# Performance work log

Measured on AMD Instinct MI355X. Metric: run time of the kernel, lower is better.

## Reference

```python
import jax, jax.numpy as jnp
import numpy as np

B, HH, WW, C = 8, 128, 128, 128
NH = 4          # total heads; each branch uses NH//2
SS = 2          # split_size
EPS = 1e-5


def setup_inputs() -> dict:
    key = jax.random.key(0)
    ks = jax.random.split(key, 10)
    Ch = C // 2
    Dff = 4 * C
    return {
        "x": jax.random.normal(ks[0], (B, HH * WW, C), jnp.float32),
        "ln1_g": jnp.ones((C,), jnp.float32),
        "ln1_b": jnp.zeros((C,), jnp.float32),
        "w_qkv": jax.random.normal(ks[1], (3 * C, C), jnp.float32) * 0.02,
        "w_proj": jax.random.normal(ks[2], (C, C), jnp.float32) * 0.02,
        "b_proj": jnp.zeros((C,), jnp.float32),
        "conv_w0": jax.random.normal(ks[3], (Ch, 1, 3, 3), jnp.float32) * 0.02,
        "conv_b0": jnp.zeros((Ch,), jnp.float32),
        "conv_w1": jax.random.normal(ks[4], (Ch, 1, 3, 3), jnp.float32) * 0.02,
        "conv_b1": jnp.zeros((Ch,), jnp.float32),
        "ln2_g": jnp.ones((C,), jnp.float32),
        "ln2_b": jnp.zeros((C,), jnp.float32),
        "w1": jax.random.normal(ks[5], (Dff, C), jnp.float32) * 0.02,
        "b1": jnp.zeros((Dff,), jnp.float32),
        "w2": jax.random.normal(ks[6], (C, Dff), jnp.float32) * 0.02,
        "b2": jnp.zeros((C,), jnp.float32),
        "H": HH,
        "W": WW,
    }


def _layernorm(x, g, b):
    m = jnp.mean(x, axis=-1, keepdims=True)
    v = jnp.mean(jnp.square(x - m), axis=-1, keepdims=True)
    return (x - m) * jax.lax.rsqrt(v + EPS) * g + b


def _cswin_branch(q, k, v, conv_w, conv_b, H, W, H_sp, W_sp, heads):
    """q,k,v: [B, H*W, Ch] -> [B, H*W, Ch] cross-shaped-window LePE attention."""
    Bq, L, Ch = q.shape
    hd = Ch // heads
    T = H_sp * W_sp
    nh, nw = H // H_sp, W // W_sp

    def to_win(t):  # [B,L,Ch] -> [nW*B, heads, T, hd]
        t = t.reshape(Bq, nh, H_sp, nw, W_sp, Ch).transpose(0, 1, 3, 2, 4, 5)
        return t.reshape(-1, T, heads, hd).transpose(0, 2, 1, 3)

    qw, kw = to_win(q), to_win(k)

    # v as window images [nW*B, Ch, H_sp, W_sp] for depthwise LePE conv
    vimg = v.reshape(Bq, nh, H_sp, nw, W_sp, Ch).transpose(0, 1, 3, 5, 2, 4)
    vimg = vimg.reshape(-1, Ch, H_sp, W_sp)
    lepe = jax.lax.conv_general_dilated(
        vimg, conv_w, window_strides=(1, 1), padding="SAME",
        feature_group_count=Ch,
        dimension_numbers=("NCHW", "OIHW", "NCHW"),
    ) + conv_b[None, :, None, None]
    lepe = lepe.reshape(-1, heads, hd, T).transpose(0, 1, 3, 2)  # [nW*B,h,T,hd]
    vw = vimg.reshape(-1, heads, hd, T).transpose(0, 1, 3, 2)

    scale = hd ** -0.5
    attn = jnp.einsum("whtd,whsd->whts", qw * scale, kw)
    attn = jax.nn.softmax(attn, axis=-1)
    out = jnp.einsum("whts,whsd->whtd", attn, vw) + lepe  # [nW*B,h,T,hd]

    out = out.transpose(0, 2, 1, 3).reshape(-1, T, Ch)
    out = out.reshape(Bq, nh, nw, H_sp, W_sp, Ch).transpose(0, 1, 3, 2, 4, 5)
    return out.reshape(Bq, H * W, Ch)


def reference(x, ln1_g, ln1_b, w_qkv, w_proj, b_proj, conv_w0, conv_b0,
              conv_w1, conv_b1, ln2_g, ln2_b, w1, b1, w2, b2, H, W):
    Bx, L, Cx = x.shape
    Ch = Cx // 2
    heads = NH // 2

    img = _layernorm(x, ln1_g, ln1_b)
    qkv = (img @ w_qkv.T).reshape(Bx, L, 3, Cx)
    q, k, v = qkv[:, :, 0, :], qkv[:, :, 1, :], qkv[:, :, 2, :]

    # idx=0: horizontal stripes (H_sp=H, W_sp=SS); idx=1: vertical (H_sp=SS, W_sp=W)
    x1 = _cswin_branch(q[..., :Ch], k[..., :Ch], v[..., :Ch],
                       conv_w0, conv_b0, H, W, H, SS, heads)
    x2 = _cswin_branch(q[..., Ch:], k[..., Ch:], v[..., Ch:],
                       conv_w1, conv_b1, H, W, SS, W, heads)
    att = jnp.concatenate([x1, x2], axis=2)
    att = att @ w_proj.T + b_proj

    x = x + att
    h = _layernorm(x, ln2_g, ln2_b)
    h = jax.nn.gelu(h @ w1.T + b1, approximate=False) @ w2.T + b2
    return x + h
```

## Files before the change

### kernel.cpp

```cpp
#include <hip/hip_runtime.h>
#include <cstddef>


#define LDIM 16384
#define NTOK 131072
#define PLANE ((size_t)NTOK * 128)

typedef __attribute__((ext_vector_type(8))) short bf16x8;
typedef __attribute__((ext_vector_type(4))) float f32x4;

__device__ __forceinline__ unsigned short f2bf(float f) {
  union { float f; unsigned int i; } u; u.f = f;
  unsigned int r = u.i + 0x7fffu + ((u.i >> 16) & 1u);
  return (unsigned short)(r >> 16);
}
__device__ __forceinline__ float bflo(unsigned int u) {
  union { unsigned int i; float f; } x; x.i = u << 16; return x.f;
}
__device__ __forceinline__ float bfhi(unsigned int u) {
  union { unsigned int i; float f; } x; x.i = u & 0xffff0000u; return x.f;
}
__device__ __forceinline__ unsigned int pk(float a, float b) {
  return (unsigned)f2bf(a) | ((unsigned)f2bf(b) << 16);
}

__device__ __forceinline__ void async16(const unsigned short* g, unsigned short* l) {
  __builtin_amdgcn_global_load_lds(
      (const __attribute__((address_space(1))) unsigned int*)g,
      (__attribute__((address_space(3))) unsigned int*)l, 16, 0, 0);
}

__device__ __forceinline__ void wait_lgkm0() {
  asm volatile("s_waitcnt lgkmcnt(0)" ::: "memory");
  __builtin_amdgcn_sched_barrier(0);
}
__device__ __forceinline__ void wait_vm0() {
  asm volatile("s_waitcnt vmcnt(0)" ::: "memory");
  __builtin_amdgcn_sched_barrier(0);
}
__device__ __forceinline__ void barrier_lgkm() {
  asm volatile("s_waitcnt lgkmcnt(0)" ::: "memory");
  __builtin_amdgcn_s_barrier();
  __builtin_amdgcn_sched_barrier(0);
}

__device__ __forceinline__ bf16x8 fragS(const unsigned short* base, int row, int c) {
  return *(const bf16x8*)(base + row * 128 + ((c ^ (row & 7)) << 3));
}

__device__ __forceinline__ void stageS128(const unsigned short* __restrict__ src, int rowStride,
                                          unsigned short* dst, int tid) {
  const int lane = tid & 63, wv = tid >> 6;
  #pragma unroll
  for (int i = 0; i < 8; i++) {
    const int base = i * 256 + wv * 64;
    const int f = base + lane;
    const int row = f >> 4, cs = f & 15, cg = cs ^ (row & 7);
    async16(src + (size_t)row * rowStride + (cg << 3), dst + (size_t)base * 8);
  }
}

__device__ __forceinline__ void stageS64(const unsigned short* __restrict__ src,
                                         unsigned short* dst, int tid) {
  const int lane = tid & 63, wv = tid >> 6;
  #pragma unroll
  for (int i = 0; i < 4; i++) {
    const int base = i * 256 + wv * 64;
    const int f = base + lane;
    const int row = f >> 4, cs = f & 15, cg = cs ^ (row & 7);
    async16(src + (size_t)row * 128 + (cg << 3), dst + (size_t)base * 8);
  }
}

__device__ __forceinline__ void stageW32(const unsigned short* __restrict__ src, int rowStride,
                                         unsigned short* dstRegion, int lane) {
  #pragma unroll
  for (int i = 0; i < 8; i++) {
    const int rowLocal = i * 4 + (lane >> 4);
    const int cs = lane & 15, cg = cs ^ (rowLocal & 7);
    async16(src + (size_t)rowLocal * rowStride + (cg << 3), dstRegion + i * 512);
  }
}

__device__ __forceinline__ void gemmS(const unsigned short* As, const unsigned short* Bs,
                                      f32x4 acc[4][4], int wm, int wn, int q, int r) {
  #pragma unroll
  for (int kc = 0; kc < 4; kc++) {
    bf16x8 a[4], b[4];
    #pragma unroll
    for (int mt = 0; mt < 4; mt++) a[mt] = fragS(As, wm * 64 + mt * 16 + r, kc * 4 + q);
    #pragma unroll
    for (int nt = 0; nt < 4; nt++) b[nt] = fragS(Bs, wn * 64 + nt * 16 + r, kc * 4 + q);
    #pragma unroll
    for (int mt = 0; mt < 4; mt++)
      #pragma unroll
      for (int nt = 0; nt < 4; nt++)
        acc[mt][nt] = __builtin_amdgcn_mfma_f32_16x16x32_bf16(a[mt], b[nt], acc[mt][nt], 0, 0, 0);
  }
}

__device__ __forceinline__ void storeC(f32x4 acc[4][4], unsigned short* Cs,
                                       unsigned short* __restrict__ dst, int dstStride, int tid) {
  const int wv = tid >> 6, lane = tid & 63, q = lane >> 4, r = lane & 15;
  const int wm = wv & 1, wn = wv >> 1;
  #pragma unroll
  for (int mt = 0; mt < 4; mt++)
    #pragma unroll
    for (int nt = 0; nt < 4; nt++) {
      const int col = wn * 64 + nt * 16 + r;
      #pragma unroll
      for (int rg = 0; rg < 4; rg++) {
        const int row = wm * 64 + mt * 16 + q * 4 + rg;
        Cs[row * 128 + ((((col >> 3) ^ (row & 7)) << 3) | (col & 7))] = f2bf(acc[mt][nt][rg]);
      }
    }
  __syncthreads();
  #pragma unroll
  for (int i = 0; i < 8; i++) {
    const int f = tid + i * 256;
    const int row = f >> 4, cs = f & 15, cg = cs ^ (row & 7);
    *(uint4*)(dst + (size_t)row * dstStride + (cg << 3)) = *(const uint4*)(Cs + row * 128 + cs * 8);
  }
}

__device__ __forceinline__ float gelu_t(float x) {
  const float y = -2.3022083f * (x + 0.044715f * x * x * x);
  const float p = __builtin_amdgcn_exp2f(y);
  return x * __builtin_amdgcn_rcpf(1.f + p);
}

__global__ void k_prep(const float* __restrict__ wq, const float* __restrict__ wp,
                       const float* __restrict__ w1, const float* __restrict__ w2,
                       unsigned short* __restrict__ wb)
{
  const int id = blockIdx.x * 256 + threadIdx.x;
  const float* src; int off;
  if (id < 12288)      { src = wq; off = id; }
  else if (id < 16384) { src = wp; off = id - 12288; }
  else if (id < 32768) { src = w1; off = id - 16384; }
  else                 { src = w2; off = id - 32768; }
  const float4 v = *(const float4*)(src + (size_t)off * 4);
  uint2 u; u.x = pk(v.x, v.y); u.y = pk(v.z, v.w);
  *(uint2*)(wb + (size_t)id * 4) = u;
}

__global__ __launch_bounds__(256, 2) void k_ln_qkv(
    const float* __restrict__ x, const float* __restrict__ g, const float* __restrict__ bb,
    const unsigned short* __restrict__ wqkvb, unsigned short* __restrict__ qkv)
{
  __shared__ unsigned short xs[128 * 128];
  __shared__ unsigned short ws[128 * 128];
  __shared__ float redS[128][2], redQ[128][2];
  const int tid = threadIdx.x;
  const long m0 = (long)blockIdx.x * 128;
  {
    const int m = tid >> 1, hf = tid & 1;
    const float4* xg = (const float4*)(x + (size_t)(m0 + m) * 128 + hf * 64);
    float4 xv[16];
    #pragma unroll
    for (int i = 0; i < 16; i++) xv[i] = xg[i];
    float s1 = 0.f, s2 = 0.f;
    #pragma unroll
    for (int i = 0; i < 16; i++) {
      s1 += xv[i].x + xv[i].y + xv[i].z + xv[i].w;
      s2 += xv[i].x * xv[i].x + xv[i].y * xv[i].y + xv[i].z * xv[i].z + xv[i].w * xv[i].w;
    }
    redS[m][hf] = s1; redQ[m][hf] = s2;
    __syncthreads();
    const float mean = (redS[m][0] + redS[m][1]) * (1.f / 128.f);
    const float var  = (redQ[m][0] + redQ[m][1]) * (1.f / 128.f) - mean * mean;
    const float rs = rsqrtf(var + 1e-5f);
    const float4* g4 = (const float4*)(g + hf * 64);
    const float4* b4 = (const float4*)(bb + hf * 64);
    #pragma unroll
    for (int i = 0; i < 8; i++) {
      float4 v0 = xv[2 * i], v1 = xv[2 * i + 1];
      float4 g0 = g4[2 * i], g1 = g4[2 * i + 1], p0 = b4[2 * i], p1 = b4[2 * i + 1];
      uint4 u;
      u.x = pk((v0.x - mean) * rs * g0.x + p0.x, (v0.y - mean) * rs * g0.y + p0.y);
      u.y = pk((v0.z - mean) * rs * g0.z + p0.z, (v0.w - mean) * rs * g0.w + p0.w);
      u.z = pk((v1.x - mean) * rs * g1.x + p1.x, (v1.y - mean) * rs * g1.y + p1.y);
      u.w = pk((v1.z - mean) * rs * g1.z + p1.z, (v1.w - mean) * rs * g1.w + p1.w);
      const int c = hf * 8 + i;
      *(uint4*)&xs[m * 128 + ((c ^ (m & 7)) << 3)] = u;
    }
  }
  const int lane = tid & 63, q = lane >> 4, r = lane & 15;
  const int wv = tid >> 6, wm = wv & 1, wn = wv >> 1;
  for (int nc = 0; nc < 3; nc++) {
    __syncthreads();
    stageS128(wqkvb + (size_t)nc * 16384, 128, ws, tid);
    __syncthreads();
    f32x4 acc[4][4];
    #pragma unroll
    for (int a = 0; a < 4; a++)
      #pragma unroll
      for (int b = 0; b < 4; b++) acc[a][b] = f32x4{0.f, 0.f, 0.f, 0.f};
    gemmS(xs, ws, acc, wm, wn, q, r);
    __syncthreads();
    storeC(acc, ws, qkv + (size_t)nc * PLANE + (size_t)m0 * 128, 128, tid);
  }
}

__global__ __launch_bounds__(256, 2) void k_attn(
    const unsigned short* __restrict__ qkv,
    const float* __restrict__ conv_w0, const float* __restrict__ conv_b0,
    const float* __restrict__ conv_w1, const float* __restrict__ conv_b1,
    unsigned short* __restrict__ att)
{
  __shared__ unsigned short Kt[256][40];
  __shared__ unsigned short Vt[32][264];
  __shared__ unsigned short Ps[4][64][72];
  const unsigned short* kpl = qkv + PLANE;
  const unsigned short* vpl = qkv + 2 * PLANE;
  const int t = threadIdx.x;
  const int win = blockIdx.x, head = blockIdx.y, br = blockIdx.z;
  const int bimg = win >> 6, widx = win & 63;
  const int c0 = br * 64 + head * 32;
  const int lgWs = (br == 0) ? 1 : 7;
  const int Wsm1 = (1 << lgWs) - 1;
  const long base = (long)bimg * LDIM + ((br == 0) ? widx * 2 : widx * 256);

  {
    const long tj = base + (long)(t >> lgWs) * 128 + (t & Wsm1);
    const uint4* kp = (const uint4*)(kpl + (size_t)tj * 128 + c0);
    uint4 k0v = kp[0], k1v = kp[1], k2v = kp[2], k3v = kp[3];
    *(uint4*)&Kt[t][0]  = k0v;  *(uint4*)&Kt[t][8]  = k1v;
    *(uint4*)&Kt[t][16] = k2v;  *(uint4*)&Kt[t][24] = k3v;
    const uint4* vp = (const uint4*)(vpl + (size_t)tj * 128 + c0);
    uint4 vv[4] = {vp[0], vp[1], vp[2], vp[3]};
    const unsigned short* vs = (const unsigned short*)vv;
    #pragma unroll
    for (int d = 0; d < 32; d++) Vt[d][t] = vs[d];
  }
  const int wave = t >> 6, lane = t & 63, q = lane >> 4, r = lane & 15;
  const int qbase = wave * 64;
  bf16x8 qf[4];
  #pragma unroll
  for (int mt = 0; mt < 4; mt++) {
    const int row = qbase + mt * 16 + r;
    const long tok = base + (long)(row >> lgWs) * 128 + (row & Wsm1);
    qf[mt] = *(const bf16x8*)(qkv + (size_t)tok * 128 + c0 + q * 8);
  }
  __syncthreads();

  const float factor = 0.17677669529663687f * 1.44269504088896341f;
  f32x4 Oacc[4][2];
  float psum[4][4];
  #pragma unroll
  for (int mt = 0; mt < 4; mt++) {
    Oacc[mt][0] = f32x4{0.f, 0.f, 0.f, 0.f};
    Oacc[mt][1] = f32x4{0.f, 0.f, 0.f, 0.f};
    #pragma unroll
    for (int rg = 0; rg < 4; rg++) psum[mt][rg] = 0.f;
  }

  for (int kc = 0; kc < 4; kc++) {
    bf16x8 kb[4];
    #pragma unroll
    for (int nt = 0; nt < 4; nt++) kb[nt] = *(const bf16x8*)&Kt[kc * 64 + nt * 16 + r][q * 8];
    f32x4 s[4][4];
    #pragma unroll
    for (int mt = 0; mt < 4; mt++)
      #pragma unroll
      for (int nt = 0; nt < 4; nt++) {
        f32x4 z = f32x4{0.f, 0.f, 0.f, 0.f};
        s[mt][nt] = __builtin_amdgcn_mfma_f32_16x16x32_bf16(qf[mt], kb[nt], z, 0, 0, 0);
      }
    #pragma unroll
    for (int mt = 0; mt < 4; mt++)
      #pragma unroll
      for (int nt = 0; nt < 4; nt++)
        #pragma unroll
        for (int rg = 0; rg < 4; rg++) {
          const float p = __builtin_amdgcn_exp2f(s[mt][nt][rg] * factor);
          psum[mt][rg] += p;
          Ps[wave][mt * 16 + q * 4 + rg][nt * 16 + r] = f2bf(p);
        }
    #pragma unroll
    for (int kst = 0; kst < 2; kst++) {
      bf16x8 pa[4], vb[2];
      #pragma unroll
      for (int mt = 0; mt < 4; mt++) pa[mt] = *(const bf16x8*)&Ps[wave][mt * 16 + r][kst * 32 + q * 8];
      #pragma unroll
      for (int nto = 0; nto < 2; nto++) vb[nto] = *(const bf16x8*)&Vt[nto * 16 + r][kc * 64 + kst * 32 + q * 8];
      #pragma unroll
      for (int mt = 0; mt < 4; mt++)
        #pragma unroll
        for (int nto = 0; nto < 2; nto++)
          Oacc[mt][nto] = __builtin_amdgcn_mfma_f32_16x16x32_bf16(pa[mt], vb[nto], Oacc[mt][nto], 0, 0, 0);
    }
  }

  #pragma unroll
  for (int mt = 0; mt < 4; mt++)
    #pragma unroll
    for (int rg = 0; rg < 4; rg++) {
      float v = psum[mt][rg];
      v += __shfl_xor(v, 1); v += __shfl_xor(v, 2);
      v += __shfl_xor(v, 4); v += __shfl_xor(v, 8);
      psum[mt][rg] = __builtin_amdgcn_rcpf(v);
    }

  const float* cw = br ? conv_w1 : conv_w0;
  const float* cb = br ? conv_b1 : conv_b0;
  float wle[2][9], ble[2];
  #pragma unroll
  for (int nto = 0; nto < 2; nto++) {
    const int ch = head * 32 + nto * 16 + r;
    ble[nto] = cb[ch];
    #pragma unroll
    for (int tp = 0; tp < 9; tp++) wle[nto][tp] = cw[ch * 9 + tp];
  }
  const int WsW = 1 << lgWs;
  const int HsW = 256 >> lgWs;

  #pragma unroll
  for (int mt = 0; mt < 4; mt++)
    #pragma unroll
    for (int rg = 0; rg < 4; rg++) {
      const int row = qbase + mt * 16 + q * 4 + rg;
      const int ii = row >> lgWs, jj = row & Wsm1;
      const long tok = base + (long)ii * 128 + jj;
      float lep0 = ble[0], lep1 = ble[1];
      #pragma unroll
      for (int di = -1; di <= 1; di++) {
        if ((unsigned)(ii + di) >= (unsigned)HsW) continue;
        #pragma unroll
        for (int dj = -1; dj <= 1; dj++) {
          if ((unsigned)(jj + dj) >= (unsigned)WsW) continue;
          const int nb = row + di * WsW + dj;
          const int tap = (di + 1) * 3 + (dj + 1);
          lep0 = fmaf(bflo(Vt[r][nb]),      wle[0][tap], lep0);
          lep1 = fmaf(bflo(Vt[16 + r][nb]), wle[1][tap], lep1);
        }
      }
      const float pr = psum[mt][rg];
      att[(size_t)tok * 128 + c0 + r]      = f2bf(Oacc[mt][0][rg] * pr + lep0);
      att[(size_t)tok * 128 + c0 + 16 + r] = f2bf(Oacc[mt][1][rg] * pr + lep1);
    }
}

__global__ __launch_bounds__(256, 2) void k_projmlp(
    const unsigned short* __restrict__ att, const unsigned short* __restrict__ wprojb,
    const float* __restrict__ b_proj, const float* __restrict__ x,
    const float* __restrict__ g, const float* __restrict__ bb,
    const unsigned short* __restrict__ w1b, const unsigned short* __restrict__ w2b,
    const float* __restrict__ b1, const float* __restrict__ b2,
    float* __restrict__ out)
{
  __shared__ unsigned short hs[64 * 128];
  __shared__ unsigned short xs[64 * 128];
  __shared__ unsigned short ws[128 * 128];
  __shared__ float redS[64][4], redQ[64][4];
  const int tid = threadIdx.x;
  const long m0 = (long)blockIdx.x * 64;
  const int lane = tid & 63, q = lane >> 4, r = lane & 15, wv = tid >> 6;
  unsigned short* wsW = ws + (size_t)wv * 32 * 128;

  stageS64(att + (size_t)m0 * 128, hs, tid);
  stageW32(wprojb + (size_t)(wv * 32) * 128, 128, wsW, lane);

  float xv[4][2][4];
  #pragma unroll
  for (int mt = 0; mt < 4; mt++)
    #pragma unroll
    for (int nt = 0; nt < 2; nt++) {
      const int col = wv * 32 + nt * 16 + r;
      #pragma unroll
      for (int rg = 0; rg < 4; rg++)
        xv[mt][nt][rg] = x[(size_t)(m0 + mt * 16 + q * 4 + rg) * 128 + col];
    }
  float bpv[2], gv[2], bv2[2], b1v[4][2], b2v[2];
  #pragma unroll
  for (int nt = 0; nt < 2; nt++) {
    const int col = wv * 32 + nt * 16 + r;
    bpv[nt] = b_proj[col]; gv[nt] = g[col]; bv2[nt] = bb[col]; b2v[nt] = b2[col];
    #pragma unroll
    for (int nc = 0; nc < 4; nc++) b1v[nc][nt] = b1[nc * 128 + col];
  }
  __syncthreads();

  f32x4 xres[4][2];
  #pragma unroll
  for (int mt = 0; mt < 4; mt++) { xres[mt][0] = f32x4{0.f,0.f,0.f,0.f}; xres[mt][1] = f32x4{0.f,0.f,0.f,0.f}; }
  #pragma unroll
  for (int kc = 0; kc < 4; kc++) {
    bf16x8 a[4], b[2];
    #pragma unroll
    for (int mt = 0; mt < 4; mt++) a[mt] = fragS(hs, mt * 16 + r, kc * 4 + q);
    #pragma unroll
    for (int nt = 0; nt < 2; nt++) b[nt] = fragS(ws, wv * 32 + nt * 16 + r, kc * 4 + q);
    #pragma unroll
    for (int mt = 0; mt < 4; mt++)
      #pragma unroll
      for (int nt = 0; nt < 2; nt++)
        xres[mt][nt] = __builtin_amdgcn_mfma_f32_16x16x32_bf16(a[mt], b[nt], xres[mt][nt], 0, 0, 0);
  }
  wait_lgkm0();
  stageW32(w1b + (size_t)(wv * 32) * 128, 128, wsW, lane);

  #pragma unroll
  for (int mt = 0; mt < 4; mt++)
    #pragma unroll
    for (int nt = 0; nt < 2; nt++)
      #pragma unroll
      for (int rg = 0; rg < 4; rg++)
        xres[mt][nt][rg] += xv[mt][nt][rg] + bpv[nt];

  #pragma unroll
  for (int mt = 0; mt < 4; mt++)
    #pragma unroll
    for (int rg = 0; rg < 4; rg++) {
      float s1 = xres[mt][0][rg] + xres[mt][1][rg];
      float s2 = xres[mt][0][rg] * xres[mt][0][rg] + xres[mt][1][rg] * xres[mt][1][rg];
      s1 += __shfl_xor(s1, 1); s1 += __shfl_xor(s1, 2); s1 += __shfl_xor(s1, 4); s1 += __shfl_xor(s1, 8);
      s2 += __shfl_xor(s2, 1); s2 += __shfl_xor(s2, 2); s2 += __shfl_xor(s2, 4); s2 += __shfl_xor(s2, 8);
      if (r == 0) { const int row = mt * 16 + q * 4 + rg; redS[row][wv] = s1; redQ[row][wv] = s2; }
    }
  barrier_lgkm();
  #pragma unroll
  for (int mt = 0; mt < 4; mt++)
    #pragma unroll
    for (int rg = 0; rg < 4; rg++) {
      const int row = mt * 16 + q * 4 + rg;
      const float s1 = redS[row][0] + redS[row][1] + redS[row][2] + redS[row][3];
      const float s2 = redQ[row][0] + redQ[row][1] + redQ[row][2] + redQ[row][3];
      const float mean = s1 * (1.f / 128.f);
      const float var  = s2 * (1.f / 128.f) - mean * mean;
      const float rs = rsqrtf(var + 1e-5f);
      #pragma unroll
      for (int nt = 0; nt < 2; nt++) {
        const int col = wv * 32 + nt * 16 + r;
        const float v = (xres[mt][nt][rg] - mean) * rs * gv[nt] + bv2[nt];
        xs[row * 128 + ((((col >> 3) ^ (row & 7)) << 3) | (col & 7))] = f2bf(v);
      }
    }
  barrier_lgkm();

  f32x4 oacc[4][2];
  #pragma unroll
  for (int mt = 0; mt < 4; mt++) { oacc[mt][0] = f32x4{0.f,0.f,0.f,0.f}; oacc[mt][1] = f32x4{0.f,0.f,0.f,0.f}; }

  for (int nc = 0; nc < 4; nc++) {
    wait_vm0();
    bf16x8 b1f[4][2];
    #pragma unroll
    for (int kc = 0; kc < 4; kc++)
      #pragma unroll
      for (int nt = 0; nt < 2; nt++)
        b1f[kc][nt] = fragS(ws, wv * 32 + nt * 16 + r, kc * 4 + q);
    wait_lgkm0();
    stageW32(w2b + (size_t)(wv * 32) * 512 + nc * 128, 512, wsW, lane);
    f32x4 h[4][2];
    #pragma unroll
    for (int mt = 0; mt < 4; mt++) { h[mt][0] = f32x4{0.f,0.f,0.f,0.f}; h[mt][1] = f32x4{0.f,0.f,0.f,0.f}; }
    #pragma unroll
    for (int kc = 0; kc < 4; kc++) {
      bf16x8 a[4];
      #pragma unroll
      for (int mt = 0; mt < 4; mt++) a[mt] = fragS(xs, mt * 16 + r, kc * 4 + q);
      #pragma unroll
      for (int mt = 0; mt < 4; mt++)
        #pragma unroll
        for (int nt = 0; nt < 2; nt++)
          h[mt][nt] = __builtin_amdgcn_mfma_f32_16x16x32_bf16(a[mt], b1f[kc][nt], h[mt][nt], 0, 0, 0);
    }
    barrier_lgkm();
    #pragma unroll
    for (int mt = 0; mt < 4; mt++)
      #pragma unroll
      for (int nt = 0; nt < 2; nt++) {
        const int col = wv * 32 + nt * 16 + r;
        const float bv = b1v[nc][nt];
        #pragma unroll
        for (int rg = 0; rg < 4; rg++) {
          const int rw = mt * 16 + q * 4 + rg;
          hs[rw * 128 + ((((col >> 3) ^ (rw & 7)) << 3) | (col & 7))] = f2bf(gelu_t(h[mt][nt][rg] + bv));
        }
      }
    barrier_lgkm();
    wait_vm0();
    bf16x8 b2f[4][2];
    #pragma unroll
    for (int kc = 0; kc < 4; kc++)
      #pragma unroll
      for (int nt = 0; nt < 2; nt++)
        b2f[kc][nt] = fragS(ws, wv * 32 + nt * 16 + r, kc * 4 + q);
    wait_lgkm0();
    if (nc < 3)
      stageW32(w1b + (size_t)((nc + 1) * 128 + wv * 32) * 128, 128, wsW, lane);
    #pragma unroll
    for (int kc = 0; kc < 4; kc++) {
      bf16x8 a[4];
      #pragma unroll
      for (int mt = 0; mt < 4; mt++) a[mt] = fragS(hs, mt * 16 + r, kc * 4 + q);
      #pragma unroll
      for (int mt = 0; mt < 4; mt++)
        #pragma unroll
        for (int nt = 0; nt < 2; nt++)
          oacc[mt][nt] = __builtin_amdgcn_mfma_f32_16x16x32_bf16(a[mt], b2f[kc][nt], oacc[mt][nt], 0, 0, 0);
    }
  }
  #pragma unroll
  for (int mt = 0; mt < 4; mt++)
    #pragma unroll
    for (int nt = 0; nt < 2; nt++) {
      const float bv = b2v[nt];
      const int col = wv * 32 + nt * 16 + r;
      #pragma unroll
      for (int rg = 0; rg < 4; rg++) {
        const size_t idx = (size_t)(m0 + mt * 16 + q * 4 + rg) * 128 + col;
        out[idx] = xres[mt][nt][rg] + bv + oacc[mt][nt][rg];
      }
    }
}

extern "C" void kernel_launch(void* const* d_in, const int* in_sizes, int n_in,
                              void* d_out, int out_size, void* d_ws, size_t ws_size,
                              hipStream_t stream) {
  const float* x       = (const float*)d_in[0];
  const float* ln1_g   = (const float*)d_in[1];
  const float* ln1_b   = (const float*)d_in[2];
  const float* w_qkv   = (const float*)d_in[3];
  const float* w_proj  = (const float*)d_in[4];
  const float* b_proj  = (const float*)d_in[5];
  const float* conv_w0 = (const float*)d_in[6];
  const float* conv_b0 = (const float*)d_in[7];
  const float* conv_w1 = (const float*)d_in[8];
  const float* conv_b1 = (const float*)d_in[9];
  const float* ln2_g   = (const float*)d_in[10];
  const float* ln2_b   = (const float*)d_in[11];
  const float* w1      = (const float*)d_in[12];
  const float* b1      = (const float*)d_in[13];
  const float* w2      = (const float*)d_in[14];
  const float* b2      = (const float*)d_in[15];
  float* out = (float*)d_out;

  unsigned short* qkv = (unsigned short*)d_ws;
  unsigned short* att = qkv;
  unsigned short* wb  = qkv + 3 * PLANE;
  unsigned short* wqkvb  = wb;
  unsigned short* wprojb = wb + 49152;
  unsigned short* w1b    = wb + 65536;
  unsigned short* w2b    = wb + 131072;

  k_prep<<<dim3(192), 256, 0, stream>>>(w_qkv, w_proj, w1, w2, wb);
  k_ln_qkv<<<dim3(NTOK / 128), 256, 0, stream>>>(x, ln1_g, ln1_b, wqkvb, qkv);
  k_attn<<<dim3(512, 2, 2), 256, 0, stream>>>(qkv, conv_w0, conv_b0, conv_w1, conv_b1, att);
  k_projmlp<<<dim3(NTOK / 64), 256, 0, stream>>>(att, wprojb, b_proj, x, ln2_g, ln2_b,
                                                 w1b, w2b, b1, b2, out);
}
```

Measured before the change: 345.2 us.

## Pipeline per-wave QKV weight staging and add MFMA priority hints

Restructures the LN+QKV kernel so each wave stages only its own 32-row weight slice asynchronously. The first slice is prefetched before the layernorm, and the next slice loads while the current GEMM runs, replacing the block-wide stage/sync/gemm/storeC sequence. Outputs are written straight from registers as packed bf16 pairs, with no shared-memory epilogue. It also wraps MFMA loops in several kernels with s_setprio so matrix work gets issue priority. The cost is more accumulator registers (8x2 tiles per wave) and narrower, less coalesced global stores.

After: 358.2 us. 3.8% more time.

```diff
diff --git a/kernel.cpp b/kernel.cpp
--- a/kernel.cpp
+++ b/kernel.cpp
@@ -38,6 +38,10 @@
   asm volatile("s_waitcnt vmcnt(0)" ::: "memory");
   __builtin_amdgcn_sched_barrier(0);
 }
+__device__ __forceinline__ void wait_vm16() {
+  asm volatile("s_waitcnt vmcnt(16)" ::: "memory");
+  __builtin_amdgcn_sched_barrier(0);
+}
 __device__ __forceinline__ void barrier_lgkm() {
   asm volatile("s_waitcnt lgkmcnt(0)" ::: "memory");
   __builtin_amdgcn_s_barrier();
@@ -46,18 +50,6 @@
 
 __device__ __forceinline__ bf16x8 fragS(const unsigned short* base, int row, int c) {
   return *(const bf16x8*)(base + row * 128 + ((c ^ (row & 7)) << 3));
-}
-
-__device__ __forceinline__ void stageS128(const unsigned short* __restrict__ src, int rowStride,
-                                          unsigned short* dst, int tid) {
-  const int lane = tid & 63, wv = tid >> 6;
-  #pragma unroll
-  for (int i = 0; i < 8; i++) {
-    const int base = i * 256 + wv * 64;
-    const int f = base + lane;
-    const int row = f >> 4, cs = f & 15, cg = cs ^ (row & 7);
-    async16(src + (size_t)row * rowStride + (cg << 3), dst + (size_t)base * 8);
-  }
 }
 
 __device__ __forceinline__ void stageS64(const unsigned short* __restrict__ src,
@@ -79,47 +71,6 @@
     const int rowLocal = i * 4 + (lane >> 4);
     const int cs = lane & 15, cg = cs ^ (rowLocal & 7);
     async16(src + (size_t)rowLocal * rowStride + (cg << 3), dstRegion + i * 512);
-  }
-}
-
-__device__ __forceinline__ void gemmS(const unsigned short* As, const unsigned short* Bs,
-                                      f32x4 acc[4][4], int wm, int wn, int q, int r) {
-  #pragma unroll
-  for (int kc = 0; kc < 4; kc++) {
-    bf16x8 a[4], b[4];
-    #pragma unroll
-    for (int mt = 0; mt < 4; mt++) a[mt] = fragS(As, wm * 64 + mt * 16 + r, kc * 4 + q);
-    #pragma unroll
-    for (int nt = 0; nt < 4; nt++) b[nt] = fragS(Bs, wn * 64 + nt * 16 + r, kc * 4 + q);
-    #pragma unroll
-    for (int mt = 0; mt < 4; mt++)
-      #pragma unroll
-      for (int nt = 0; nt < 4; nt++)
-        acc[mt][nt] = __builtin_amdgcn_mfma_f32_16x16x32_bf16(a[mt], b[nt], acc[mt][nt], 0, 0, 0);
-  }
-}
-
-__device__ __forceinline__ void storeC(f32x4 acc[4][4], unsigned short* Cs,
-                                       unsigned short* __restrict__ dst, int dstStride, int tid) {
-  const int wv = tid >> 6, lane = tid & 63, q = lane >> 4, r = lane & 15;
-  const int wm = wv & 1, wn = wv >> 1;
-  #pragma unroll
-  for (int mt = 0; mt < 4; mt++)
-    #pragma unroll
-    for (int nt = 0; nt < 4; nt++) {
-      const int col = wn * 64 + nt * 16 + r;
-      #pragma unroll
-      for (int rg = 0; rg < 4; rg++) {
-        const int row = wm * 64 + mt * 16 + q * 4 + rg;
-        Cs[row * 128 + ((((col >> 3) ^ (row & 7)) << 3) | (col & 7))] = f2bf(acc[mt][nt][rg]);
-      }
-    }
-  __syncthreads();
-  #pragma unroll
-  for (int i = 0; i < 8; i++) {
-    const int f = tid + i * 256;
-    const int row = f >> 4, cs = f & 15, cg = cs ^ (row & 7);
-    *(uint4*)(dst + (size_t)row * dstStride + (cg << 3)) = *(const uint4*)(Cs + row * 128 + cs * 8);
   }
 }
 
@@ -153,6 +104,11 @@
   __shared__ float redS[128][2], redQ[128][2];
   const int tid = threadIdx.x;
   const long m0 = (long)blockIdx.x * 128;
+  const int lane = tid & 63, q = lane >> 4, r = lane & 15, wv = tid >> 6;
+  unsigned short* wsW = ws + (size_t)wv * 32 * 128;
+
+  stageW32(wqkvb + (size_t)(wv * 32) * 128, 128, wsW, lane);
+
   {
     const int m = tid >> 1, hf = tid & 1;
     const float4* xg = (const float4*)(x + (size_t)(m0 + m) * 128 + hf * 64);
@@ -166,7 +122,7 @@
       s2 += xv[i].x * xv[i].x + xv[i].y * xv[i].y + xv[i].z * xv[i].z + xv[i].w * xv[i].w;
     }
     redS[m][hf] = s1; redQ[m][hf] = s2;
-    __syncthreads();
+    barrier_lgkm();
     const float mean = (redS[m][0] + redS[m][1]) * (1.f / 128.f);
     const float var  = (redQ[m][0] + redQ[m][1]) * (1.f / 128.f) - mean * mean;
     const float rs = rsqrtf(var + 1e-5f);
@@ -185,20 +141,45 @@
       *(uint4*)&xs[m * 128 + ((c ^ (m & 7)) << 3)] = u;
     }
   }
-  const int lane = tid & 63, q = lane >> 4, r = lane & 15;
-  const int wv = tid >> 6, wm = wv & 1, wn = wv >> 1;
+  barrier_lgkm();
+
   for (int nc = 0; nc < 3; nc++) {
-    __syncthreads();
-    stageS128(wqkvb + (size_t)nc * 16384, 128, ws, tid);
-    __syncthreads();
-    f32x4 acc[4][4];
-    #pragma unroll
-    for (int a = 0; a < 4; a++)
-      #pragma unroll
-      for (int b = 0; b < 4; b++) acc[a][b] = f32x4{0.f, 0.f, 0.f, 0.f};
-    gemmS(xs, ws, acc, wm, wn, q, r);
-    __syncthreads();
-    storeC(acc, ws, qkv + (size_t)nc * PLANE + (size_t)m0 * 128, 128, tid);
+    if (nc == 0) wait_vm0(); else wait_vm16();
+    bf16x8 wf[4][2];
+    #pragma unroll
+    for (int kc = 0; kc < 4; kc++)
+      #pragma unroll
+      for (int nt = 0; nt < 2; nt++)
+        wf[kc][nt] = fragS(ws, wv * 32 + nt * 16 + r, kc * 4 + q);
+    wait_lgkm0();
+    if (nc < 2)
+      stageW32(wqkvb + (size_t)((nc + 1) * 128 + wv * 32) * 128, 128, wsW, lane);
+    f32x4 acc[8][2];
+    #pragma unroll
+    for (int mt = 0; mt < 8; mt++) { acc[mt][0] = f32x4{0.f,0.f,0.f,0.f}; acc[mt][1] = f32x4{0.f,0.f,0.f,0.f}; }
+    __builtin_amdgcn_s_setprio(1);
+    #pragma unroll
+    for (int kc = 0; kc < 4; kc++) {
+      bf16x8 xf[8];
+      #pragma unroll
+      for (int mt = 0; mt < 8; mt++) xf[mt] = fragS(xs, mt * 16 + r, kc * 4 + q);
+      #pragma unroll
+      for (int mt = 0; mt < 8; mt++)
+        #pragma unroll
+        for (int nt = 0; nt < 2; nt++)
+          acc[mt][nt] = __builtin_amdgcn_mfma_f32_16x16x32_bf16(wf[kc][nt], xf[mt], acc[mt][nt], 0, 0, 0);
+    }
+    __builtin_amdgcn_s_setprio(0);
+    unsigned short* dst = qkv + (size_t)nc * PLANE + (size_t)m0 * 128;
+    #pragma unroll
+    for (int mt = 0; mt < 8; mt++)
+      #pragma unroll
+      for (int nt = 0; nt < 2; nt++) {
+        uint2 u;
+        u.x = pk(acc[mt][nt][0], acc[mt][nt][1]);
+        u.y = pk(acc[mt][nt][2], acc[mt][nt][3]);
+        *(uint2*)(dst + (size_t)(mt * 16 + r) * 128 + wv * 32 + nt * 16 + q * 4) = u;
+      }
   }
 }
 
@@ -260,6 +241,7 @@
     #pragma unroll
     for (int nt = 0; nt < 4; nt++) kb[nt] = *(const bf16x8*)&Kt[kc * 64 + nt * 16 + r][q * 8];
     f32x4 s[4][4];
+    __builtin_amdgcn_s_setprio(1);
     #pragma unroll
     for (int mt = 0; mt < 4; mt++)
       #pragma unroll
@@ -267,6 +249,7 @@
         f32x4 z = f32x4{0.f, 0.f, 0.f, 0.f};
         s[mt][nt] = __builtin_amdgcn_mfma_f32_16x16x32_bf16(qf[mt], kb[nt], z, 0, 0, 0);
       }
+    __builtin_amdgcn_s_setprio(0);
     #pragma unroll
     for (int mt = 0; mt < 4; mt++)
       #pragma unroll
@@ -284,11 +267,13 @@
       for (int mt = 0; mt < 4; mt++) pa[mt] = *(const bf16x8*)&Ps[wave][mt * 16 + r][kst * 32 + q * 8];
       #pragma unroll
       for (int nto = 0; nto < 2; nto++) vb[nto] = *(const bf16x8*)&Vt[nto * 16 + r][kc * 64 + kst * 32 + q * 8];
+      __builtin_amdgcn_s_setprio(1);
       #pragma unroll
       for (int mt = 0; mt < 4; mt++)
         #pragma unroll
         for (int nto = 0; nto < 2; nto++)
           Oacc[mt][nto] = __builtin_amdgcn_mfma_f32_16x16x32_bf16(pa[mt], vb[nto], Oacc[mt][nto], 0, 0, 0);
+      __builtin_amdgcn_s_setprio(0);
     }
   }
 
@@ -384,6 +369,7 @@
   f32x4 xres[4][2];
   #pragma unroll
   for (int mt = 0; mt < 4; mt++) { xres[mt][0] = f32x4{0.f,0.f,0.f,0.f}; xres[mt][1] = f32x4{0.f,0.f,0.f,0.f}; }
+  __builtin_amdgcn_s_setprio(1);
   #pragma unroll
   for (int kc = 0; kc < 4; kc++) {
     bf16x8 a[4], b[2];
@@ -397,6 +383,7 @@
       for (int nt = 0; nt < 2; nt++)
         xres[mt][nt] = __builtin_amdgcn_mfma_f32_16x16x32_bf16(a[mt], b[nt], xres[mt][nt], 0, 0, 0);
   }
+  __builtin_amdgcn_s_setprio(0);
   wait_lgkm0();
   stageW32(w1b + (size_t)(wv * 32) * 128, 128, wsW, lane);
 
@@ -455,6 +442,7 @@
     f32x4 h[4][2];
     #pragma unroll
     for (int mt = 0; mt < 4; mt++) { h[mt][0] = f32x4{0.f,0.f,0.f,0.f}; h[mt][1] = f32x4{0.f,0.f,0.f,0.f}; }
+    __builtin_amdgcn_s_setprio(1);
     #pragma unroll
     for (int kc = 0; kc < 4; kc++) {
       bf16x8 a[4];
@@ -466,6 +454,7 @@
         for (int nt = 0; nt < 2; nt++)
           h[mt][nt] = __builtin_amdgcn_mfma_f32_16x16x32_bf16(a[mt], b1f[kc][nt], h[mt][nt], 0, 0, 0);
     }
+    __builtin_amdgcn_s_setprio(0);
     barrier_lgkm();
     #pragma unroll
     for (int mt = 0; mt < 4; mt++)
@@ -490,6 +479,7 @@
     wait_lgkm0();
     if (nc < 3)
       stageW32(w1b + (size_t)((nc + 1) * 128 + wv * 32) * 128, 128, wsW, lane);
+    __builtin_amdgcn_s_setprio(1);
     #pragma unroll
     for (int kc = 0; kc < 4; kc++) {
       bf16x8 a[4];
@@ -501,6 +491,7 @@
         for (int nt = 0; nt < 2; nt++)
           oacc[mt][nt] = __builtin_amdgcn_mfma_f32_16x16x32_bf16(a[mt], b2f[kc][nt], oacc[mt][nt], 0, 0, 0);
     }
+    __builtin_amdgcn_s_setprio(0);
   }
   #pragma unroll
   for (int mt = 0; mt < 4; mt++)
```

## Split projection-MLP block into 8 waves over a 2x4 row/column grid

Applied to the files above, without the earlier changes.

Launches the fused proj+LN2+MLP kernel with 512 threads, so each wave now handles 32 rows by 32 columns instead of 64 by 32. This halves per-wave accumulator registers and doubles resident waves to hide LDS and global latency. The two row-groups share the weight slice in shared memory, so barriers replace some local waits. Pairs of waves redundantly issue the same weight staging copies, and there is more barrier synchronization.

Result: slower. 392.0 us (+13.6%).

```diff
diff --git a/kernel.cpp b/kernel.cpp
--- a/kernel.cpp
+++ b/kernel.cpp
@@ -60,12 +60,12 @@
   }
 }
 
-__device__ __forceinline__ void stageS64(const unsigned short* __restrict__ src,
-                                         unsigned short* dst, int tid) {
+__device__ __forceinline__ void stageS64b(const unsigned short* __restrict__ src,
+                                          unsigned short* dst, int tid) {
   const int lane = tid & 63, wv = tid >> 6;
   #pragma unroll
-  for (int i = 0; i < 4; i++) {
-    const int base = i * 256 + wv * 64;
+  for (int i = 0; i < 2; i++) {
+    const int base = i * 512 + wv * 64;
     const int f = base + lane;
     const int row = f >> 4, cs = f & 15, cg = cs ^ (row & 7);
     async16(src + (size_t)row * 128 + (cg << 3), dst + (size_t)base * 8);
@@ -341,7 +341,7 @@
     }
 }
 
-__global__ __launch_bounds__(256, 2) void k_projmlp(
+__global__ __launch_bounds__(512, 4) void k_projmlp(
     const unsigned short* __restrict__ att, const unsigned short* __restrict__ wprojb,
     const float* __restrict__ b_proj, const float* __restrict__ x,
     const float* __restrict__ g, const float* __restrict__ bb,
@@ -356,52 +356,50 @@
   const int tid = threadIdx.x;
   const long m0 = (long)blockIdx.x * 64;
   const int lane = tid & 63, q = lane >> 4, r = lane & 15, wv = tid >> 6;
-  unsigned short* wsW = ws + (size_t)wv * 32 * 128;
-
-  stageS64(att + (size_t)m0 * 128, hs, tid);
-  stageW32(wprojb + (size_t)(wv * 32) * 128, 128, wsW, lane);
-
-  float xv[4][2][4];
-  #pragma unroll
-  for (int mt = 0; mt < 4; mt++)
+  const int wm = wv >> 2, wn = wv & 3;
+  unsigned short* wsR = ws + (size_t)wn * 32 * 128;
+
+  stageS64b(att + (size_t)m0 * 128, hs, tid);
+  stageW32(wprojb + (size_t)(wn * 32) * 128, 128, wsR, lane);
+
+  float xv[2][2][4];
+  #pragma unroll
+  for (int mt = 0; mt < 2; mt++)
     #pragma unroll
     for (int nt = 0; nt < 2; nt++) {
-      const int col = wv * 32 + nt * 16 + r;
+      const int col = wn * 32 + nt * 16 + r;
       #pragma unroll
       for (int rg = 0; rg < 4; rg++)
-        xv[mt][nt][rg] = x[(size_t)(m0 + mt * 16 + q * 4 + rg) * 128 + col];
+        xv[mt][nt][rg] = x[(size_t)(m0 + wm * 32 + mt * 16 + q * 4 + rg) * 128 + col];
     }
   float bpv[2], gv[2], bv2[2], b1v[4][2], b2v[2];
   #pragma unroll
   for (int nt = 0; nt < 2; nt++) {
-    const int col = wv * 32 + nt * 16 + r;
+    const int col = wn * 32 + nt * 16 + r;
     bpv[nt] = b_proj[col]; gv[nt] = g[col]; bv2[nt] = bb[col]; b2v[nt] = b2[col];
     #pragma unroll
     for (int nc = 0; nc < 4; nc++) b1v[nc][nt] = b1[nc * 128 + col];
   }
   __syncthreads();
 
-  f32x4 xres[4][2];
-  #pragma unroll
-  for (int mt = 0; mt < 4; mt++) { xres[mt][0] = f32x4{0.f,0.f,0.f,0.f}; xres[mt][1] = f32x4{0.f,0.f,0.f,0.f}; }
+  f32x4 xres[2][2];
+  #pragma unroll
+  for (int mt = 0; mt < 2; mt++) { xres[mt][0] = f32x4{0.f,0.f,0.f,0.f}; xres[mt][1] = f32x4{0.f,0.f,0.f,0.f}; }
   #pragma unroll
   for (int kc = 0; kc < 4; kc++) {
-    bf16x8 a[4], b[2];
-    #pragma unroll
-    for (int mt = 0; mt < 4; mt++) a[mt] = fragS(hs, mt * 16 + r, kc * 4 + q);
-    #pragma unroll
-    for (int nt = 0; nt < 2; nt++) b[nt] = fragS(ws, wv * 32 + nt * 16 + r, kc * 4 + q);
-    #pragma unroll
-    for (int mt = 0; mt < 4; mt++)
+    bf16x8 a[2], b[2];
+    #pragma unroll
+    for (int mt = 0; mt < 2; mt++) a[mt] = fragS(hs, wm * 32 + mt * 16 + r, kc * 4 + q);
+    #pragma unroll
+    for (int nt = 0; nt < 2; nt++) b[nt] = fragS(wsR, nt * 16 + r, kc * 4 + q);
+    #pragma unroll
+    for (int mt = 0; mt < 2; mt++)
       #pragma unroll
       for (int nt = 0; nt < 2; nt++)
         xres[mt][nt] = __builtin_amdgcn_mfma_f32_16x16x32_bf16(a[mt], b[nt], xres[mt][nt], 0, 0, 0);
   }
-  wait_lgkm0();
-  stageW32(w1b + (size_t)(wv * 32) * 128, 128, wsW, lane);
-
-  #pragma unroll
-  for (int mt = 0; mt < 4; mt++)
+  #pragma unroll
+  for (int mt = 0; mt < 2; mt++)
     #pragma unroll
     for (int nt = 0; nt < 2; nt++)
       #pragma unroll
@@ -409,21 +407,22 @@
         xres[mt][nt][rg] += xv[mt][nt][rg] + bpv[nt];
 
   #pragma unroll
-  for (int mt = 0; mt < 4; mt++)
+  for (int mt = 0; mt < 2; mt++)
     #pragma unroll
     for (int rg = 0; rg < 4; rg++) {
       float s1 = xres[mt][0][rg] + xres[mt][1][rg];
       float s2 = xres[mt][0][rg] * xres[mt][0][rg] + xres[mt][1][rg] * xres[mt][1][rg];
       s1 += __shfl_xor(s1, 1); s1 += __shfl_xor(s1, 2); s1 += __shfl_xor(s1, 4); s1 += __shfl_xor(s1, 8);
       s2 += __shfl_xor(s2, 1); s2 += __shfl_xor(s2, 2); s2 += __shfl_xor(s2, 4); s2 += __shfl_xor(s2, 8);
-      if (r == 0) { const int row = mt * 16 + q * 4 + rg; redS[row][wv] = s1; redQ[row][wv] = s2; }
+      if (r == 0) { const int row = wm * 32 + mt * 16 + q * 4 + rg; redS[row][wn] = s1; redQ[row][wn] = s2; }
     }
   barrier_lgkm();
-  #pragma unroll
-  for (int mt = 0; mt < 4; mt++)
+  stageW32(w1b + (size_t)(wn * 32) * 128, 128, wsR, lane);
+  #pragma unroll
+  for (int mt = 0; mt < 2; mt++)
     #pragma unroll
     for (int rg = 0; rg < 4; rg++) {
-      const int row = mt * 16 + q * 4 + rg;
+      const int row = wm * 32 + mt * 16 + q * 4 + rg;
       const float s1 = redS[row][0] + redS[row][1] + redS[row][2] + redS[row][3];
       const float s2 = redQ[row][0] + redQ[row][1] + redQ[row][2] + redQ[row][3];
       const float mean = s1 * (1.f / 128.f);
@@ -431,16 +430,16 @@
       const float rs = rsqrtf(var + 1e-5f);
       #pragma unroll
       for (int nt = 0; nt < 2; nt++) {
-        const int col = wv * 32 + nt * 16 + r;
+        const int col = wn * 32 + nt * 16 + r;
         const float v = (xres[mt][nt][rg] - mean) * rs * gv[nt] + bv2[nt];
         xs[row * 128 + ((((col >> 3) ^ (row & 7)) << 3) | (col & 7))] = f2bf(v);
       }
     }
   barrier_lgkm();
 
-  f32x4 oacc[4][2];
-  #pragma unroll
-  for (int mt = 0; mt < 4; mt++) { oacc[mt][0] = f32x4{0.f,0.f,0.f,0.f}; oacc[mt][1] = f32x4{0.f,0.f,0.f,0.f}; }
+  f32x4 oacc[2][2];
+  #pragma unroll
+  for (int mt = 0; mt < 2; mt++) { oacc[mt][0] = f32x4{0.f,0.f,0.f,0.f}; oacc[mt][1] = f32x4{0.f,0.f,0.f,0.f}; }
 
   for (int nc = 0; nc < 4; nc++) {
     wait_vm0();
@@ -449,33 +448,32 @@
     for (int kc = 0; kc < 4; kc++)
       #pragma unroll
       for (int nt = 0; nt < 2; nt++)
-        b1f[kc][nt] = fragS(ws, wv * 32 + nt * 16 + r, kc * 4 + q);
-    wait_lgkm0();
-    stageW32(w2b + (size_t)(wv * 32) * 512 + nc * 128, 512, wsW, lane);
-    f32x4 h[4][2];
-    #pragma unroll
-    for (int mt = 0; mt < 4; mt++) { h[mt][0] = f32x4{0.f,0.f,0.f,0.f}; h[mt][1] = f32x4{0.f,0.f,0.f,0.f}; }
+        b1f[kc][nt] = fragS(wsR, nt * 16 + r, kc * 4 + q);
+    f32x4 h[2][2];
+    #pragma unroll
+    for (int mt = 0; mt < 2; mt++) { h[mt][0] = f32x4{0.f,0.f,0.f,0.f}; h[mt][1] = f32x4{0.f,0.f,0.f,0.f}; }
     #pragma unroll
     for (int kc = 0; kc < 4; kc++) {
-      bf16x8 a[4];
-      #pragma unroll
-      for (int mt = 0; mt < 4; mt++) a[mt] = fragS(xs, mt * 16 + r, kc * 4 + q);
-      #pragma unroll
-      for (int mt = 0; mt < 4; mt++)
+      bf16x8 a[2];
+      #pragma unroll
+      for (int mt = 0; mt < 2; mt++) a[mt] = fragS(xs, wm * 32 + mt * 16 + r, kc * 4 + q);
+      #pragma unroll
+      for (int mt = 0; mt < 2; mt++)
         #pragma unroll
         for (int nt = 0; nt < 2; nt++)
           h[mt][nt] = __builtin_amdgcn_mfma_f32_16x16x32_bf16(a[mt], b1f[kc][nt], h[mt][nt], 0, 0, 0);
     }
     barrier_lgkm();
-    #pragma unroll
-    for (int mt = 0; mt < 4; mt++)
+    stageW32(w2b + (size_t)(wn * 32) * 512 + nc * 128, 512, wsR, lane);
+    #pragma unroll
+    for (int mt = 0; mt < 2; mt++)
       #pragma unroll
       for (int nt = 0; nt < 2; nt++) {
-        const int col = wv * 32 + nt * 16 + r;
+        const int col = wn * 32 + nt * 16 + r;
         const float bv = b1v[nc][nt];
         #pragma unroll
         for (int rg = 0; rg < 4; rg++) {
-          const int rw = mt * 16 + q * 4 + rg;
+          const int rw = wm * 32 + mt * 16 + q * 4 + rg;
           hs[rw * 128 + ((((col >> 3) ^ (rw & 7)) << 3) | (col & 7))] = f2bf(gelu_t(h[mt][nt][rg] + bv));
         }
       }
@@ -486,31 +484,31 @@
     for (int kc = 0; kc < 4; kc++)
       #pragma unroll
       for (int nt = 0; nt < 2; nt++)
-        b2f[kc][nt] = fragS(ws, wv * 32 + nt * 16 + r, kc * 4 + q);
-    wait_lgkm0();
+        b2f[kc][nt] = fragS(wsR, nt * 16 + r, kc * 4 + q);
+    barrier_lgkm();
     if (nc < 3)
-      stageW32(w1b + (size_t)((nc + 1) * 128 + wv * 32) * 128, 128, wsW, lane);
+      stageW32(w1b + (size_t)((nc + 1) * 128 + wn * 32) * 128, 128, wsR, lane);
     #pragma unroll
     for (int kc = 0; kc < 4; kc++) {
-      bf16x8 a[4];
-      #pragma unroll
-      for (int mt = 0; mt < 4; mt++) a[mt] = fragS(hs, mt * 16 + r, kc * 4 + q);
-      #pragma unroll
-      for (int mt = 0; mt < 4; mt++)
+      bf16x8 a[2];
+      #pragma unroll
+      for (int mt = 0; mt < 2; mt++) a[mt] = fragS(hs, wm * 32 + mt * 16 + r, kc * 4 + q);
+      #pragma unroll
+      for (int mt = 0; mt < 2; mt++)
         #pragma unroll
         for (int nt = 0; nt < 2; nt++)
           oacc[mt][nt] = __builtin_amdgcn_mfma_f32_16x16x32_bf16(a[mt], b2f[kc][nt], oacc[mt][nt], 0, 0, 0);
     }
   }
   #pragma unroll
-  for (int mt = 0; mt < 4; mt++)
+  for (int mt = 0; mt < 2; mt++)
     #pragma unroll
     for (int nt = 0; nt < 2; nt++) {
       const float bv = b2v[nt];
-      const int col = wv * 32 + nt * 16 + r;
+      const int col = wn * 32 + nt * 16 + r;
       #pragma unroll
       for (int rg = 0; rg < 4; rg++) {
-        const size_t idx = (size_t)(m0 + mt * 16 + q * 4 + rg) * 128 + col;
+        const size_t idx = (size_t)(m0 + wm * 32 + mt * 16 + q * 4 + rg) * 128 + col;
         out[idx] = xres[mt][nt][rg] + bv + oacc[mt][nt][rg];
       }
     }
@@ -548,6 +546,6 @@
   k_prep<<<dim3(192), 256, 0, stream>>>(w_qkv, w_proj, w1, w2, wb);
   k_ln_qkv<<<dim3(NTOK / 128), 256, 0, stream>>>(x, ln1_g, ln1_b, wqkvb, qkv);
   k_attn<<<dim3(512, 2, 2), 256, 0, stream>>>(qkv, conv_w0, conv_b0, conv_w1, conv_b1, att);
-  k_projmlp<<<dim3(NTOK / 64), 256, 0, stream>>>(att, wprojb, b_proj, x, ln2_g, ln2_b,
+  k_projmlp<<<dim3(NTOK / 64), 512, 0, stream>>>(att, wprojb, b_proj, x, ln2_g, ln2_b,
                                                  w1b, w2b, b1, b2, out);
 }
```

## Load MLP weight fragments directly into registers with double-buffered prefetch

Applied to the files above, without the earlier changes.

In the proj+MLP kernel, weight tiles are now read straight from global memory into per-wave register fragments, with the next chunk prefetched into registers while the current one feeds the MFMAs. This removes the LDS weight-staging buffer and its explicit waitcnt points. The QKV kernel also starts staging the first weight chunk before the layernorm so the load overlaps that work. The cost is higher register pressure from two sets of eight fragments, which may lower occupancy, and uncoalesced 16-byte global reads that now rely on the cache.

Result: no change. 348.0 us (+0.8%).

```diff
diff --git a/kernel.cpp b/kernel.cpp
--- a/kernel.cpp
+++ b/kernel.cpp
@@ -17,9 +17,6 @@
 __device__ __forceinline__ float bflo(unsigned int u) {
   union { unsigned int i; float f; } x; x.i = u << 16; return x.f;
 }
-__device__ __forceinline__ float bfhi(unsigned int u) {
-  union { unsigned int i; float f; } x; x.i = u & 0xffff0000u; return x.f;
-}
 __device__ __forceinline__ unsigned int pk(float a, float b) {
   return (unsigned)f2bf(a) | ((unsigned)f2bf(b) << 16);
 }
@@ -30,14 +27,6 @@
       (__attribute__((address_space(3))) unsigned int*)l, 16, 0, 0);
 }
 
-__device__ __forceinline__ void wait_lgkm0() {
-  asm volatile("s_waitcnt lgkmcnt(0)" ::: "memory");
-  __builtin_amdgcn_sched_barrier(0);
-}
-__device__ __forceinline__ void wait_vm0() {
-  asm volatile("s_waitcnt vmcnt(0)" ::: "memory");
-  __builtin_amdgcn_sched_barrier(0);
-}
 __device__ __forceinline__ void barrier_lgkm() {
   asm volatile("s_waitcnt lgkmcnt(0)" ::: "memory");
   __builtin_amdgcn_s_barrier();
@@ -46,6 +35,10 @@
 
 __device__ __forceinline__ bf16x8 fragS(const unsigned short* base, int row, int c) {
   return *(const bf16x8*)(base + row * 128 + ((c ^ (row & 7)) << 3));
+}
+
+__device__ __forceinline__ bf16x8 ldw(const unsigned short* p) {
+  return *(const bf16x8*)p;
 }
 
 __device__ __forceinline__ void stageS128(const unsigned short* __restrict__ src, int rowStride,
@@ -69,16 +62,6 @@
     const int f = base + lane;
     const int row = f >> 4, cs = f & 15, cg = cs ^ (row & 7);
     async16(src + (size_t)row * 128 + (cg << 3), dst + (size_t)base * 8);
-  }
-}
-
-__device__ __forceinline__ void stageW32(const unsigned short* __restrict__ src, int rowStride,
-                                         unsigned short* dstRegion, int lane) {
-  #pragma unroll
-  for (int i = 0; i < 8; i++) {
-    const int rowLocal = i * 4 + (lane >> 4);
-    const int cs = lane & 15, cg = cs ^ (rowLocal & 7);
-    async16(src + (size_t)rowLocal * rowStride + (cg << 3), dstRegion + i * 512);
   }
 }
 
@@ -153,6 +136,9 @@
   __shared__ float redS[128][2], redQ[128][2];
   const int tid = threadIdx.x;
   const long m0 = (long)blockIdx.x * 128;
+
+  stageS128(wqkvb, 128, ws, tid);
+
   {
     const int m = tid >> 1, hf = tid & 1;
     const float4* xg = (const float4*)(x + (size_t)(m0 + m) * 128 + hf * 64);
@@ -189,8 +175,10 @@
   const int wv = tid >> 6, wm = wv & 1, wn = wv >> 1;
   for (int nc = 0; nc < 3; nc++) {
     __syncthreads();
-    stageS128(wqkvb + (size_t)nc * 16384, 128, ws, tid);
-    __syncthreads();
+    if (nc > 0) {
+      stageS128(wqkvb + (size_t)nc * 16384, 128, ws, tid);
+      __syncthreads();
+    }
     f32x4 acc[4][4];
     #pragma unroll
     for (int a = 0; a < 4; a++)
@@ -350,16 +338,20 @@
     float* __restrict__ out)
 {
   __shared__ unsigned short hs[64 * 128];
-  __shared__ unsigned short xs[64 * 128];
-  __shared__ unsigned short ws[128 * 128];
+  __shared__ unsigned short xs[64 * 128 + 16384];
   __shared__ float redS[64][4], redQ[64][4];
   const int tid = threadIdx.x;
   const long m0 = (long)blockIdx.x * 64;
   const int lane = tid & 63, q = lane >> 4, r = lane & 15, wv = tid >> 6;
-  unsigned short* wsW = ws + (size_t)wv * 32 * 128;
 
   stageS64(att + (size_t)m0 * 128, hs, tid);
-  stageW32(wprojb + (size_t)(wv * 32) * 128, 128, wsW, lane);
+
+  bf16x8 wcur[8];
+  #pragma unroll
+  for (int kc = 0; kc < 4; kc++)
+    #pragma unroll
+    for (int nt = 0; nt < 2; nt++)
+      wcur[kc * 2 + nt] = ldw(wprojb + (size_t)(wv * 32 + nt * 16 + r) * 128 + kc * 32 + q * 8);
 
   float xv[4][2][4];
   #pragma unroll
@@ -386,19 +378,21 @@
   for (int mt = 0; mt < 4; mt++) { xres[mt][0] = f32x4{0.f,0.f,0.f,0.f}; xres[mt][1] = f32x4{0.f,0.f,0.f,0.f}; }
   #pragma unroll
   for (int kc = 0; kc < 4; kc++) {
-    bf16x8 a[4], b[2];
+    bf16x8 a[4];
     #pragma unroll
     for (int mt = 0; mt < 4; mt++) a[mt] = fragS(hs, mt * 16 + r, kc * 4 + q);
     #pragma unroll
-    for (int nt = 0; nt < 2; nt++) b[nt] = fragS(ws, wv * 32 + nt * 16 + r, kc * 4 + q);
-    #pragma unroll
     for (int mt = 0; mt < 4; mt++)
       #pragma unroll
       for (int nt = 0; nt < 2; nt++)
-        xres[mt][nt] = __builtin_amdgcn_mfma_f32_16x16x32_bf16(a[mt], b[nt], xres[mt][nt], 0, 0, 0);
-  }
-  wait_lgkm0();
-  stageW32(w1b + (size_t)(wv * 32) * 128, 128, wsW, lane);
+        xres[mt][nt] = __builtin_amdgcn_mfma_f32_16x16x32_bf16(a[mt], wcur[kc * 2 + nt], xres[mt][nt], 0, 0, 0);
+  }
+  bf16x8 wnxt[8];
+  #pragma unroll
+  for (int kc = 0; kc < 4; kc++)
+    #pragma unroll
+    for (int nt = 0; nt < 2; nt++)
+      wnxt[kc * 2 + nt] = ldw(w1b + (size_t)(wv * 32 + nt * 16 + r) * 128 + kc * 32 + q * 8);
 
   #pragma unroll
   for (int mt = 0; mt < 4; mt++)
@@ -443,15 +437,13 @@
   for (int mt = 0; mt < 4; mt++) { oacc[mt][0] = f32x4{0.f,0.f,0.f,0.f}; oacc[mt][1] = f32x4{0.f,0.f,0.f,0.f}; }
 
   for (int nc = 0; nc < 4; nc++) {
-    wait_vm0();
-    bf16x8 b1f[4][2];
+    #pragma unroll
+    for (int i = 0; i < 8; i++) wcur[i] = wnxt[i];
     #pragma unroll
     for (int kc = 0; kc < 4; kc++)
       #pragma unroll
       for (int nt = 0; nt < 2; nt++)
-        b1f[kc][nt] = fragS(ws, wv * 32 + nt * 16 + r, kc * 4 + q);
-    wait_lgkm0();
-    stageW32(w2b + (size_t)(wv * 32) * 512 + nc * 128, 512, wsW, lane);
+        wnxt[kc * 2 + nt] = ldw(w2b + (size_t)(wv * 32 + nt * 16 + r) * 512 + nc * 128 + kc * 32 + q * 8);
     f32x4 h[4][2];
     #pragma unroll
     for (int mt = 0; mt < 4; mt++) { h[mt][0] = f32x4{0.f,0.f,0.f,0.f}; h[mt][1] = f32x4{0.f,0.f,0.f,0.f}; }
@@ -464,7 +456,7 @@
       for (int mt = 0; mt < 4; mt++)
         #pragma unroll
         for (int nt = 0; nt < 2; nt++)
-          h[mt][nt] = __builtin_amdgcn_mfma_f32_16x16x32_bf16(a[mt], b1f[kc][nt], h[mt][nt], 0, 0, 0);
+          h[mt][nt] = __builtin_amdgcn_mfma_f32_16x16x32_bf16(a[mt], wcur[kc * 2 + nt], h[mt][nt], 0, 0, 0);
     }
     barrier_lgkm();
     #pragma unroll
@@ -480,16 +472,15 @@
         }
       }
     barrier_lgkm();
-    wait_vm0();
-    bf16x8 b2f[4][2];
-    #pragma unroll
-    for (int kc = 0; kc < 4; kc++)
-      #pragma unroll
-      for (int nt = 0; nt < 2; nt++)
-        b2f[kc][nt] = fragS(ws, wv * 32 + nt * 16 + r, kc * 4 + q);
-    wait_lgkm0();
-    if (nc < 3)
-      stageW32(w1b + (size_t)((nc + 1) * 128 + wv * 32) * 128, 128, wsW, lane);
+    #pragma unroll
+    for (int i = 0; i < 8; i++) wcur[i] = wnxt[i];
+    if (nc < 3) {
+      #pragma unroll
+      for (int kc = 0; kc < 4; kc++)
+        #pragma unroll
+        for (int nt = 0; nt < 2; nt++)
+          wnxt[kc * 2 + nt] = ldw(w1b + (size_t)((nc + 1) * 128 + wv * 32 + nt * 16 + r) * 128 + kc * 32 + q * 8);
+    }
     #pragma unroll
     for (int kc = 0; kc < 4; kc++) {
       bf16x8 a[4];
@@ -499,7 +490,7 @@
       for (int mt = 0; mt < 4; mt++)
         #pragma unroll
         for (int nt = 0; nt < 2; nt++)
-          oacc[mt][nt] = __builtin_amdgcn_mfma_f32_16x16x32_bf16(a[mt], b2f[kc][nt], oacc[mt][nt], 0, 0, 0);
+          oacc[mt][nt] = __builtin_amdgcn_mfma_f32_16x16x32_bf16(a[mt], wcur[kc * 2 + nt], oacc[mt][nt], 0, 0, 0);
     }
   }
   #pragma unroll
```
